# Performance work log

Hardware: AMD Instinct MI355X
Metric: run time of the kernel (lower is better)

The kernel has to match this reference:

```python
import jax, jax.numpy as jnp
import numpy as np

B, NW, NS, SL = 32, 500, 50, 40
EMB, HID, VOCAB, E = 300, 150, 50000, 563200
N = B * (NW + NS)
MAXPOS = 512


def _sinusoid(n_pos, d):
    pos = np.arange(n_pos)[:, None].astype(np.float64)
    i = np.arange(d)[None, :]
    ang = pos / np.power(10000.0, 2 * (i // 2) / d)
    tab = np.zeros((n_pos, d))
    tab[:, 0::2] = np.sin(ang[:, 0::2])
    tab[:, 1::2] = np.cos(ang[:, 1::2])
    tab[0] = 0.0  # padding_idx=0
    return jnp.asarray(tab, dtype=jnp.float32)

_POS_TAB = _sinusoid(MAXPOS + 1, EMB)


def setup_inputs():
    keys = iter(jax.random.split(jax.random.key(0), 48))
    def nrm(shape, s=0.05):
        return jax.random.normal(next(keys), shape, dtype=jnp.float32) * s
    inp = {}
    inp["x"] = jax.random.randint(next(keys), (B, NW), 0, VOCAB, dtype=jnp.int32)
    inp["sent_x"] = jax.random.randint(next(keys), (B, NS, SL), 0, VOCAB, dtype=jnp.int32)
    inp["edge_index"] = jax.random.randint(next(keys), (2, E), 0, N, dtype=jnp.int32)
    inp["embed_table"] = nrm((VOCAB, EMB)).at[0].set(0.0)  # padding_idx=0
    for h in range(2, 8):
        inp["conv_w%d" % h] = nrm((50, 1, h, EMB))
        inp["conv_b%d" % h] = nrm((50,))
    inp["cnn_proj_w"] = nrm((HID, EMB)); inp["cnn_proj_b"] = nrm((HID,))
    inp["lstm_w_ih_l0"] = nrm((2, 4 * HID, HID)); inp["lstm_w_hh_l0"] = nrm((2, 4 * HID, HID))
    inp["lstm_b_ih_l0"] = nrm((2, 4 * HID)); inp["lstm_b_hh_l0"] = nrm((2, 4 * HID))
    inp["lstm_w_ih_l1"] = nrm((2, 4 * HID, 2 * HID)); inp["lstm_w_hh_l1"] = nrm((2, 4 * HID, HID))
    inp["lstm_b_ih_l1"] = nrm((2, 4 * HID)); inp["lstm_b_hh_l1"] = nrm((2, 4 * HID))
    inp["lstm_proj_w"] = nrm((HID, 2 * HID)); inp["lstm_proj_b"] = nrm((HID,))
    inp["gc0_w"] = nrm((HID, EMB)); inp["gc0_b"] = nrm((HID,))
    inp["gc1_w"] = nrm((HID, HID)); inp["gc1_b"] = nrm((HID,))
    inp["gc2_w"] = nrm((HID, HID)); inp["gc2_b"] = nrm((HID,))
    return inp


def _forward(x, sent_x, edge_index, embed_table, conv_ws, conv_bs,
             cnn_proj_w, cnn_proj_b, w_ih0, w_hh0, b_ih0, b_hh0,
             w_ih1, w_hh1, b_ih1, b_hh1, lstm_proj_w, lstm_proj_b,
             gc0_w, gc0_b, gc1_w, gc1_b, gc2_w, gc2_b):
    Bsz, S, L = sent_x.shape
    Nn = Bsz * S
    emb_words = embed_table[x]                                   # [B, NW, EMB]
    tok = embed_table[sent_x].reshape(Nn, L, EMB)                # [Nn, L, EMB]
    sentlen = (sent_x != 0).sum(-1).reshape(Nn)                  # token count per sentence
    a = jnp.arange(L)
    input_pos = jnp.where(a[None, :] < sentlen[:, None], a[None, :] + 1, 0)
    enc = tok + _POS_TAB[input_pos]
    # CNN ngram features: conv heights 2..7, full-width kernels == windowed matmuls
    feats = []
    for w, b in zip(conv_ws, conv_bs):
        h = w.shape[2]
        acc = b + sum(jnp.einsum('nld,od->nlo', enc[:, k:L - h + 1 + k, :], w[:, 0, k, :]) for k in range(h))
        feats.append(jnp.max(jax.nn.relu(acc), axis=1))          # [Nn, 50]
    ngram = jnp.concatenate(feats, axis=1)                        # [Nn, 300]
    snode_pos = jnp.tile(jnp.arange(S), Bsz)
    cnn_feat = ((ngram + _POS_TAB[snode_pos]) @ cnn_proj_w.T + cnn_proj_b).reshape(Bsz, S, HID)
    glen = (sent_x[:, :, 0] != 0).sum(-1)                         # valid sentence count per graph

    def lstm_dir(xs, w_ih, w_hh, bias):
        def step(carry, xt):
            hh, cc = carry
            g = xt @ w_ih.T + hh @ w_hh.T + bias
            i, f, gg, o = jnp.split(g, 4, axis=-1)
            cc = jax.nn.sigmoid(f) * cc + jax.nn.sigmoid(i) * jnp.tanh(gg)
            hh = jax.nn.sigmoid(o) * jnp.tanh(cc)
            return (hh, cc), hh
        z = jnp.zeros((xs.shape[0], HID), xs.dtype)
        _, hs = jax.lax.scan(step, (z, z), jnp.swapaxes(xs, 0, 1))
        return jnp.swapaxes(hs, 0, 1)

    def rev_within(xs):
        # reverse only the first glen[b] steps (packed-sequence semantics)
        T = xs.shape[1]; t = jnp.arange(T)
        idx = jnp.where(t[None, :] < glen[:, None], glen[:, None] - 1 - t[None, :], t[None, :])
        return jnp.take_along_axis(xs, idx[:, :, None], axis=1)

    def bidir(xs, w_ih, w_hh, b_i, b_h):
        f = lstm_dir(xs, w_ih[0], w_hh[0], b_i[0] + b_h[0])
        r = rev_within(lstm_dir(rev_within(xs), w_ih[1], w_hh[1], b_i[1] + b_h[1]))
        return jnp.concatenate([f, r], axis=-1)

    h1 = bidir(cnn_feat, w_ih0, w_hh0, b_ih0, b_hh0)
    h2 = bidir(h1, w_ih1, w_hh1, b_ih1, b_hh1)
    mask = (jnp.arange(S)[None, :] < glen[:, None]).astype(h2.dtype)[:, :, None]
    lstm_feat = (h2 * mask) @ lstm_proj_w.T + lstm_proj_b
    sent_out = jnp.concatenate([cnn_feat, lstm_feat], axis=-1)    # [B, S, 300]
    nodes = jnp.concatenate([emb_words, sent_out], axis=1)        # [B, NW+S, 300]
    nodes = (nodes @ gc0_w.T + gc0_b).reshape(-1, HID)            # [N, 150]
    Nt = nodes.shape[0]
    loop = jnp.arange(Nt, dtype=edge_index.dtype)
    src = jnp.concatenate([edge_index[0], loop])                  # add self-loops
    dst = jnp.concatenate([edge_index[1], loop])
    deg = jax.ops.segment_sum(jnp.ones(src.shape[0], nodes.dtype), dst, num_segments=Nt)
    dis = jnp.where(deg > 0, jax.lax.rsqrt(deg), 0.0)
    norm = (dis[src] * dis[dst])[:, None]

    def gcn(xin, w, bias):
        xw = xin @ w.T
        return jax.ops.segment_sum(xw[src] * norm, dst, num_segments=Nt) + bias

    h = jax.nn.elu(gcn(nodes, gc1_w, gc1_b))
    # F.dropout with training=False -> identity
    return gcn(h, gc2_w, gc2_b), emb_words


def reference(x, sent_x, edge_index, embed_table, conv_w2, conv_b2, conv_w3, conv_b3,
              conv_w4, conv_b4, conv_w5, conv_b5, conv_w6, conv_b6, conv_w7, conv_b7,
              cnn_proj_w, cnn_proj_b, lstm_w_ih_l0, lstm_w_hh_l0, lstm_b_ih_l0, lstm_b_hh_l0,
              lstm_w_ih_l1, lstm_w_hh_l1, lstm_b_ih_l1, lstm_b_hh_l1, lstm_proj_w, lstm_proj_b,
              gc0_w, gc0_b, gc1_w, gc1_b, gc2_w, gc2_b):
    conv_ws = [conv_w2, conv_w3, conv_w4, conv_w5, conv_w6, conv_w7]
    conv_bs = [conv_b2, conv_b3, conv_b4, conv_b5, conv_b6, conv_b7]
    return _forward(x, sent_x, edge_index, embed_table, conv_ws, conv_bs,
                    cnn_proj_w, cnn_proj_b, lstm_w_ih_l0, lstm_w_hh_l0, lstm_b_ih_l0, lstm_b_hh_l0,
                    lstm_w_ih_l1, lstm_w_hh_l1, lstm_b_ih_l1, lstm_b_hh_l1, lstm_proj_w, lstm_proj_b,
                    gc0_w, gc0_b, gc1_w, gc1_b, gc2_w, gc2_b)
```

## Files before the change

### kernel.cpp

```cpp
#include <hip/hip_runtime.h>
#include <stdint.h>
#include <math.h>

#define EDGES 563200
#define NNODES 17600
#define OUT0SZ 2640000
#define MROWS 64000
#define MPAD  64016
#define KSTRIDE 2112

typedef _Float16 h2 __attribute__((ext_vector_type(2)));
typedef _Float16 h4 __attribute__((ext_vector_type(4)));
typedef _Float16 v8h __attribute__((ext_vector_type(8)));
typedef float v4f __attribute__((ext_vector_type(4)));

__device__ __forceinline__ float sigm(float x){ return 1.f / (1.f + expf(-x)); }

__device__ __forceinline__ float fdot2_(h2 a, h2 b, float c){
#if __has_builtin(__builtin_amdgcn_fdot2)
  return __builtin_amdgcn_fdot2(a, b, c, false);
#else
  return c + (float)a.x * (float)b.x + (float)a.y * (float)b.y;
#endif
}

__global__ void gcnk_postab(float* __restrict__ pos){
  int idx = blockIdx.x * 256 + threadIdx.x;
  if (idx >= 513 * 300) return;
  int p = idx / 300, i = idx - p * 300;
  float v = 0.f;
  if (p != 0){
    double expo = (double)(2 * (i / 2)) / 300.0;
    double ang = (double)p / pow(10000.0, expo);
    v = (float)((i & 1) ? cos(ang) : sin(ang));
  }
  pos[idx] = v;
}

__global__ void gcnk_prep(const int* __restrict__ sx, int* __restrict__ sentlen,
                          int* __restrict__ glen){
  int tid = blockIdx.x * 256 + threadIdx.x;
  if (tid < 1600){
    int c = 0;
    for (int j = 0; j < 40; j++) c += (sx[tid * 40 + j] != 0);
    sentlen[tid] = c;
  } else if (tid < 1632){
    int b = tid - 1600, c = 0;
    for (int s = 0; s < 50; s++) c += (sx[b * 2000 + s * 40] != 0);
    glen[b] = c;
  }
}

__global__ void gcnk_rowmap(const int* __restrict__ glen, int* __restrict__ rowmap){
  int i = blockIdx.x * 256 + threadIdx.x;
  if (i >= 1600) return;
  int b = i / 50, t = i - b * 50, g = glen[b];
  rowmap[i] = b * 50 + ((t < g) ? (g - 1 - t) : t);
}

__global__ void gcnk_embw(const int* __restrict__ x, const float* __restrict__ tab,
                          float4* __restrict__ out){
  int idx = blockIdx.x * 256 + threadIdx.x;
  if (idx >= 16000 * 75) return;
  int row = idx / 75, q = idx - row * 75;
  const float4* t = (const float4*)tab;
  out[idx] = t[x[row] * 75 + q];
}

__global__ void gcnk_zeroi(unsigned int* __restrict__ p, int n){
  int i = blockIdx.x * 256 + threadIdx.x;
  if (i < n) p[i] = 0u;
}

__global__ void gcnk_ench(const int* __restrict__ sx, const float* __restrict__ tab,
                          const float* __restrict__ pos, const int* __restrict__ sentlen,
                          _Float16* __restrict__ ench){
  int idx = blockIdx.x * 256 + threadIdx.x;
  if (idx >= MPAD * 75) return;
  int row = idx / 75, q = idx - row * 75;
  int d = q * 4;
  h4 o; o[0] = (_Float16)0.f; o[1] = (_Float16)0.f; o[2] = (_Float16)0.f; o[3] = (_Float16)0.f;
  if (row < MROWS){
    int n = row / 40, l = row - n * 40;
    int tok = sx[n * 40 + l];
    int p = (l < sentlen[n]) ? (l + 1) : 0;
    float4 a = *(const float4*)(tab + (size_t)tok * 300 + d);
    float4 b = *(const float4*)(pos + (size_t)p * 300 + d);
    o[0] = (_Float16)(a.x + b.x); o[1] = (_Float16)(a.y + b.y);
    o[2] = (_Float16)(a.z + b.z); o[3] = (_Float16)(a.w + b.w);
  }
  *(h4*)(ench + (size_t)row * 300 + d) = o;
}

__global__ void gcnk_bpack(const float* w2, const float* w3, const float* w4,
                           const float* w5, const float* w6, const float* w7,
                           const float* c2, const float* c3, const float* c4,
                           const float* c5, const float* c6, const float* c7,
                           _Float16* __restrict__ Bp, float* __restrict__ bias_p){
  int idx = blockIdx.x * 256 + threadIdx.x;
  if (idx < 2 * 160 * KSTRIDE){
    int n = idx / KSTRIDE, kk = idx - n * KSTRIDE;
    int g = n / 160, c = n - g * 160;
    _Float16 v = (_Float16)0.f;
    if (c < 150){
      int H = 3 * g + 2 + c / 50, o = c % 50;
      if (kk < 300 * H){
        const float* w;
        switch (H){ case 2: w = w2; break; case 3: w = w3; break;
                    case 4: w = w4; break; case 5: w = w5; break;
                    case 6: w = w6; break; default: w = w7; break; }
        v = (_Float16)w[o * 300 * H + kk];
      }
    }
    Bp[idx] = v;
  }
  if (idx < 320){
    int g = idx / 160, c = idx - g * 160;
    float bv = 0.f;
    if (c < 150){
      int H = 3 * g + 2 + c / 50, o = c % 50;
      const float* cbp;
      switch (H){ case 2: cbp = c2; break; case 3: cbp = c3; break;
                  case 4: cbp = c4; break; case 5: cbp = c5; break;
                  case 6: cbp = c6; break; default: cbp = c7; break; }
      bv = cbp[o];
    }
    bias_p[idx] = bv;
  }
}

__global__ __launch_bounds__(256)
void gcnk_convmfma(const _Float16* __restrict__ A, const _Float16* __restrict__ Bp,
                   const float* __restrict__ bias_p, unsigned int* __restrict__ ngram_u){
  __shared__ __align__(16) char smem[23040];
  _Float16* As = (_Float16*)smem;
  _Float16* Bs = (_Float16*)(smem + 10240);
  float* Cs = (float*)smem;
  const int tid = threadIdx.x;
  const int m0 = blockIdx.x * 128;
  const int grp = blockIdx.y;
  const _Float16* Bg = Bp + (size_t)grp * 160 * KSTRIDE;
  const int kmax = grp ? 2112 : 1216;
  const int w = tid >> 6, lane = tid & 63;
  const int wm = (w >> 1) * 64, wn = (w & 1) * 80;
  const int fm = lane & 15, fq = lane >> 4;
  v4f acc[4][5] = {};

  for (int kc = 0; kc < kmax; kc += 32){
    #pragma unroll
    for (int j = 0; j < 4; j++){
      int u = tid + 256 * j;
      int row = u >> 3, part = u & 7;
      uint2 v = *(const uint2*)(A + (size_t)(m0 + row) * 300 + kc + part * 4);
      *(uint2*)(As + row * 40 + part * 4) = v;
    }
    #pragma unroll
    for (int j = 0; j < 5; j++){
      int u = tid + 256 * j;
      int row = u >> 3, part = u & 7;
      uint2 v = *(const uint2*)(Bg + (size_t)row * KSTRIDE + kc + part * 4);
      *(uint2*)(Bs + row * 40 + part * 4) = v;
    }
    __syncthreads();
    v8h af[4], bf[5];
    #pragma unroll
    for (int mt = 0; mt < 4; mt++)
      af[mt] = *(const v8h*)(As + (wm + mt * 16 + fm) * 40 + fq * 8);
    #pragma unroll
    for (int nt = 0; nt < 5; nt++)
      bf[nt] = *(const v8h*)(Bs + (wn + nt * 16 + fm) * 40 + fq * 8);
    #pragma unroll
    for (int mt = 0; mt < 4; mt++)
      #pragma unroll
      for (int nt = 0; nt < 5; nt++)
        acc[mt][nt] = __builtin_amdgcn_mfma_f32_16x16x32_f16(af[mt], bf[nt], acc[mt][nt], 0, 0, 0);
    __syncthreads();
  }

  for (int p = 0; p < 5; p++){
    __syncthreads();
    #pragma unroll
    for (int nt = 0; nt < 5; nt++){
      int cstart = wn + nt * 16;
      if ((cstart >> 5) == p){
        int co = cstart - p * 32 + fm;
        #pragma unroll
        for (int mt = 0; mt < 4; mt++)
          #pragma unroll
          for (int r = 0; r < 4; r++)
            Cs[(wm + mt * 16 + fq * 4 + r) * 33 + co] = acc[mt][nt][r];
      }
    }
    __syncthreads();
    if (tid < 128){
      int cl = tid & 31, si = tid >> 5;
      int col = p * 32 + cl;
      if (col < 150){
        int H = 3 * grp + 2 + col / 50, lh = 41 - H;
        int sent = m0 / 40 + si;
        int rlo = sent * 40; if (rlo < m0) rlo = m0;
        int rhi = sent * 40 + lh; if (rhi > m0 + 128) rhi = m0 + 128;
        if (rlo < rhi){
          float bv = bias_p[grp * 160 + col];
          float vmax = 0.f;
          for (int r = rlo; r < rhi; r++){
            float v = Cs[(r - m0) * 33 + cl] + bv;
            vmax = fmaxf(vmax, v);
          }
          atomicMax(ngram_u + sent * 300 + grp * 150 + col, __float_as_uint(vmax));
        }
      }
    }
  }
}

__global__ void gcnk_addpos(float* __restrict__ ngram, const float* __restrict__ pos){
  int idx = blockIdx.x * 256 + threadIdx.x;
  if (idx >= 1600 * 300) return;
  int row = idx / 300, d = idx - row * 300;
  ngram[idx] += pos[(row % 50) * 300 + d];
}

template<int BM, int BN, int WMT, int WNT>
__global__ __launch_bounds__(256)
void gcnk_mgemm(const float* __restrict__ A, const float* __restrict__ Wt,
                const float* __restrict__ b1, const float* __restrict__ b2,
                float* __restrict__ C, int M, int N, int K){
  __shared__ __align__(16) _Float16 As[BM * 40];
  __shared__ __align__(16) _Float16 Bs[BN * 40];
  const int tid = threadIdx.x;
  const int m0 = blockIdx.x * BM, n0 = blockIdx.y * BN;
  const int w = tid >> 6, lane = tid & 63;
  const int wm = (w >> 1) * (WMT * 16), wn = (w & 1) * (WNT * 16);
  const int fm = lane & 15, fq = lane >> 4;
  v4f acc[WMT][WNT] = {};
  const int nch = (K + 31) >> 5;
  for (int ch = 0; ch < nch; ch++){
    int kc = ch * 32;
    #pragma unroll
    for (int j = 0; j < BM / 64; j++){
      int u = tid + 256 * j;
      int row = u >> 2, cb = (u & 3) * 8;
      int gm = m0 + row, gk = kc + cb;
      v8h vv;
      if (gm < M && gk + 8 <= K){
        const float* p = A + (size_t)gm * K + gk;
        #pragma unroll
        for (int e = 0; e < 8; e++) vv[e] = (_Float16)p[e];
      } else {
        #pragma unroll
        for (int e = 0; e < 8; e++)
          vv[e] = (gm < M && gk + e < K) ? (_Float16)A[(size_t)gm * K + gk + e] : (_Float16)0.f;
      }
      *(v8h*)(As + row * 40 + cb) = vv;
    }
    {
      int row = tid >> 2, cb = (tid & 3) * 8;
      int gn = n0 + row, gk = kc + cb;
      v8h vv;
      if (gn < N && gk + 8 <= K){
        const float* p = Wt + (size_t)gn * K + gk;
        #pragma unroll
        for (int e = 0; e < 8; e++) vv[e] = (_Float16)p[e];
      } else {
        #pragma unroll
        for (int e = 0; e < 8; e++)
          vv[e] = (gn < N && gk + e < K) ? (_Float16)Wt[(size_t)gn * K + gk + e] : (_Float16)0.f;
      }
      *(v8h*)(Bs + row * 40 + cb) = vv;
    }
    __syncthreads();
    v8h af[WMT], bf[WNT];
    #pragma unroll
    for (int mt = 0; mt < WMT; mt++)
      af[mt] = *(const v8h*)(As + (wm + mt * 16 + fm) * 40 + fq * 8);
    #pragma unroll
    for (int nt = 0; nt < WNT; nt++)
      bf[nt] = *(const v8h*)(Bs + (wn + nt * 16 + fm) * 40 + fq * 8);
    #pragma unroll
    for (int mt = 0; mt < WMT; mt++)
      #pragma unroll
      for (int nt = 0; nt < WNT; nt++)
        acc[mt][nt] = __builtin_amdgcn_mfma_f32_16x16x32_f16(af[mt], bf[nt], acc[mt][nt], 0, 0, 0);
    __syncthreads();
  }
  #pragma unroll
  for (int nt = 0; nt < WNT; nt++){
    int gn = n0 + wn + nt * 16 + fm;
    if (gn >= N) continue;
    float badd = (b1 ? b1[gn] : 0.f) + (b2 ? b2[gn] : 0.f);
    #pragma unroll
    for (int mt = 0; mt < WMT; mt++)
      #pragma unroll
      for (int r = 0; r < 4; r++){
        int gm = m0 + wm + mt * 16 + fq * 4 + r;
        if (gm < M) C[(size_t)gm * N + gn] = acc[mt][nt][r] + badd;
      }
  }
}

__global__ void gcnk_permute150(float* __restrict__ dst, const float* __restrict__ src,
                                const int* __restrict__ map){
  int idx = blockIdx.x * 256 + threadIdx.x;
  if (idx >= 1600 * 150) return;
  int row = idx / 150, d = idx - row * 150;
  dst[idx] = src[map[row] * 150 + d];
}

__global__ void gcnk_concat(float* __restrict__ dst, const float* __restrict__ A,
                            const float* __restrict__ Bs, const int* __restrict__ mapA,
                            const int* __restrict__ mapB, const int* __restrict__ glen,
                            int usemask){
  int idx = blockIdx.x * 256 + threadIdx.x;
  if (idx >= 1600 * 300) return;
  int row = idx / 300, d = idx - row * 300;
  int b = row / 50, t = row - b * 50;
  float v;
  if (d < 150){ int r = mapA ? mapA[row] : row; v = A[r * 150 + d]; }
  else        { int r = mapB ? mapB[row] : row; v = Bs[r * 150 + d - 150]; }
  if (usemask && t >= glen[b]) v = 0.f;
  dst[idx] = v;
}

__global__ void gcnk_whhpack(const float* __restrict__ whh, _Float16* __restrict__ wpad){
  int idx = blockIdx.x * 256 + threadIdx.x;
  if (idx >= 1200 * 152) return;
  int row = idx / 152, col = idx - row * 152;
  wpad[idx] = (col < 150) ? (_Float16)whh[row * 150 + col] : (_Float16)0.f;
}

__global__ __launch_bounds__(640)
void gcnk_lstm(const float* __restrict__ xf, const float* __restrict__ xr,
               const _Float16* __restrict__ wpad, float* __restrict__ fo,
               float* __restrict__ ro){
  int b = blockIdx.x >> 1, dir = blockIdx.x & 1;
  const float* xih = dir ? xr : xf;
  float* out = dir ? ro : fo;
  __shared__ __align__(16) _Float16 hh[160];
  __shared__ float gates[600];
  const int tid = threadIdx.x;

  h2 w[76];
  if (tid < 600){
    const h2* wrow = (const h2*)(wpad + ((size_t)dir * 600 + tid) * 152);
    #pragma unroll
    for (int j = 0; j < 76; j++) w[j] = wrow[j];
  }
  for (int u = tid; u < 160; u += 640) hh[u] = (_Float16)0.f;
  float creg = 0.f;
  __syncthreads();

  for (int t = 0; t < 50; t++){
    if (tid < 600){
      float acc = xih[(b * 50 + t) * 600 + tid];
      #pragma unroll
      for (int j = 0; j < 19; j++){
        union { float4 f; h2 h[4]; } u;
        u.f = *(const float4*)(hh + j * 8);
        acc = fdot2_(w[4 * j + 0], u.h[0], acc);
        acc = fdot2_(w[4 * j + 1], u.h[1], acc);
        acc = fdot2_(w[4 * j + 2], u.h[2], acc);
        acc = fdot2_(w[4 * j + 3], u.h[3], acc);
      }
      gates[tid] = acc;
    }
    __syncthreads();
    if (tid < 150){
      float ig = sigm(gates[tid]);
      float fg = sigm(gates[150 + tid]);
      float gg = tanhf(gates[300 + tid]);
      float og = sigm(gates[450 + tid]);
      creg = fg * creg + ig * gg;
      float hn = og * tanhf(creg);
      hh[tid] = (_Float16)hn;
      out[(b * 50 + t) * 150 + tid] = hn;
    }
    __syncthreads();
  }
}

__global__ void gcnk_nodes_in(const int* __restrict__ x, const float* __restrict__ tab,
                              const float* __restrict__ cnnf, const float* __restrict__ lstmf,
                              float* __restrict__ out){
  int idx = blockIdx.x * 256 + threadIdx.x;
  if (idx >= NNODES * 300) return;
  int nrow = idx / 300, d = idx - nrow * 300;
  int b = nrow / 550, j = nrow - b * 550;
  float v;
  if (j < 500) v = tab[x[b * 500 + j] * 300 + d];
  else {
    int r = b * 50 + (j - 500);
    v = (d < 150) ? cnnf[r * 150 + d] : lstmf[r * 150 + d - 150];
  }
  out[idx] = v;
}

__global__ void gcnk_hist(const int* __restrict__ ei, int* __restrict__ ecnt){
  int e = blockIdx.x * 256 + threadIdx.x;
  if (e < EDGES) atomicAdd(&ecnt[ei[EDGES + e]], 1);
}

__global__ __launch_bounds__(1024)
void gcnk_scan(const int* __restrict__ ecnt, int* __restrict__ eoff,
               int* __restrict__ ecur){
  __shared__ int buf[1024];
  int tid = threadIdx.x;
  int running = 0;
  for (int c = 0; c < 18; c++){
    int i = c * 1024 + tid;
    int v = (i < NNODES) ? ecnt[i] : 0;
    buf[tid] = v;
    __syncthreads();
    for (int s = 1; s < 1024; s <<= 1){
      int t2 = (tid >= s) ? buf[tid - s] : 0;
      __syncthreads();
      buf[tid] += t2;
      __syncthreads();
    }
    int excl = running + buf[tid] - v;
    int tot = buf[1023];
    if (i < NNODES){ eoff[i] = excl; ecur[i] = excl; }
    running += tot;
    __syncthreads();
  }
}

__global__ void gcnk_scatter(const int* __restrict__ ei, int* __restrict__ ecur,
                             int* __restrict__ esrc){
  int e = blockIdx.x * 256 + threadIdx.x;
  if (e < EDGES){
    int d = ei[EDGES + e];
    int p = atomicAdd(&ecur[d], 1);
    esrc[p] = ei[e];
  }
}

__global__ void gcnk_dis2(const int* __restrict__ ecnt, float* __restrict__ dis){
  int i = blockIdx.x * 256 + threadIdx.x;
  if (i < NNODES) dis[i] = rsqrtf((float)(ecnt[i] + 1));
}

__global__ __launch_bounds__(128)
void gcnk_aggcsr(const int* __restrict__ eoff, const int* __restrict__ ecnt,
                 const int* __restrict__ esrc, const float* __restrict__ dis,
                 const float* __restrict__ xw, float* __restrict__ agg){
  int d = blockIdx.x, t = threadIdx.x;
  float dd = dis[d];
  const float* xd = xw + (size_t)d * 150;
  float a0 = xd[t] * dd;
  float a1 = (t < 22) ? xd[128 + t] * dd : 0.f;
  int beg = eoff[d], end = beg + ecnt[d];
  for (int j = beg; j < end; j++){
    int s = esrc[j];
    float ds = dis[s];
    const float* xs = xw + (size_t)s * 150;
    a0 += xs[t] * ds;
    if (t < 22) a1 += xs[128 + t] * ds;
  }
  agg[(size_t)d * 150 + t] = a0 * dd;
  if (t < 22) agg[(size_t)d * 150 + 128 + t] = a1 * dd;
}

__global__ void gcnk_elu(float* __restrict__ h, const float* __restrict__ agg,
                         const float* __restrict__ bias){
  int idx = blockIdx.x * 256 + threadIdx.x;
  if (idx >= NNODES * 150) return;
  int c = idx % 150;
  float v = agg[idx] + bias[c];
  h[idx] = (v > 0.f) ? v : expm1f(v);
}

__global__ void gcnk_out0(float* __restrict__ out, const float* __restrict__ agg,
                          const float* __restrict__ bias){
  int idx = blockIdx.x * 256 + threadIdx.x;
  if (idx >= NNODES * 150) return;
  int c = idx % 150;
  out[idx] = agg[idx] + bias[c];
}

extern "C" void kernel_launch(void* const* d_in, const int* in_sizes, int n_in,
                              void* d_out, int out_size, void* d_ws, size_t ws_size,
                              hipStream_t stream){
  (void)in_sizes; (void)n_in; (void)out_size; (void)ws_size;

  char* wsb = (char*)d_ws;
  size_t off = 0;
  auto alloc = [&](size_t bytes) -> void* {
    void* p = wsb + off;
    off = (off + bytes + 255) & ~(size_t)255;
    return p;
  };
  float* pos_tab  = (float*)alloc(513 * 300 * 4);
  int*   sentlen  = (int*)alloc(1600 * 4);
  int*   glen     = (int*)alloc(32 * 4);
  int*   rowmap   = (int*)alloc(1600 * 4);
  float* ngram    = (float*)alloc(1600 * 300 * 4);
  float* cnn_feat = (float*)alloc(1600 * 150 * 4);
  float* cnn_rev  = (float*)alloc(1600 * 150 * 4);
  float* xih_f    = (float*)alloc(1600 * 600 * 4);
  float* xih_r    = (float*)alloc(1600 * 600 * 4);
  float* f0       = (float*)alloc(1600 * 150 * 4);
  float* r0       = (float*)alloc(1600 * 150 * 4);
  float* f1       = (float*)alloc(1600 * 150 * 4);
  float* r1       = (float*)alloc(1600 * 150 * 4);
  float* h1       = (float*)alloc(1600 * 300 * 4);
  float* h1rev    = (float*)alloc(1600 * 300 * 4);
  float* hm       = (float*)alloc(1600 * 300 * 4);
  float* lstm_ft  = (float*)alloc(1600 * 150 * 4);
  float* nodes_in = (float*)alloc((size_t)NNODES * 300 * 4);
  float* nodes    = (float*)alloc((size_t)NNODES * 150 * 4);
  float* dis      = (float*)alloc(NNODES * 4);
  float* xw       = (float*)alloc((size_t)NNODES * 150 * 4);
  float* agg      = (float*)alloc((size_t)NNODES * 150 * 4);
  _Float16* ench  = (_Float16*)alloc((size_t)MPAD * 300 * 2);
  _Float16* Bp    = (_Float16*)alloc((size_t)2 * 160 * KSTRIDE * 2);
  float* bias_p   = (float*)alloc(320 * 4);
  _Float16* wpad0 = (_Float16*)alloc(1200 * 152 * 2);
  _Float16* wpad1 = (_Float16*)alloc(1200 * 152 * 2);
  int*   ecnt     = (int*)alloc(NNODES * 4);
  int*   eoff     = (int*)alloc(NNODES * 4);
  int*   ecur     = (int*)alloc(NNODES * 4);
  int*   esrc     = (int*)alloc(EDGES * 4);

  const int*   x   = (const int*)d_in[0];
  const int*   sx  = (const int*)d_in[1];
  const int*   ei  = (const int*)d_in[2];
  const float* tab = (const float*)d_in[3];
  const float *cw[6], *cb[6];
  for (int h = 0; h < 6; h++){ cw[h] = (const float*)d_in[4 + 2 * h]; cb[h] = (const float*)d_in[5 + 2 * h]; }
  const float* cnnw = (const float*)d_in[16]; const float* cnnb = (const float*)d_in[17];
  const float* wih0 = (const float*)d_in[18]; const float* whh0 = (const float*)d_in[19];
  const float* bih0 = (const float*)d_in[20]; const float* bhh0 = (const float*)d_in[21];
  const float* wih1 = (const float*)d_in[22]; const float* whh1 = (const float*)d_in[23];
  const float* bih1 = (const float*)d_in[24]; const float* bhh1 = (const float*)d_in[25];
  const float* lpw  = (const float*)d_in[26]; const float* lpb  = (const float*)d_in[27];
  const float* g0w  = (const float*)d_in[28]; const float* g0b  = (const float*)d_in[29];
  const float* g1w  = (const float*)d_in[30]; const float* g1b  = (const float*)d_in[31];
  const float* g2w  = (const float*)d_in[32]; const float* g2b  = (const float*)d_in[33];

  float* out0 = (float*)d_out;
  float4* out1 = (float4*)((float*)d_out + OUT0SZ);

  auto mgemmL = [&](const float* A, const float* W, const float* b1, const float* b2,
                    float* C, int M, int N, int K){
    dim3 g((M + 127) / 128, (N + 63) / 64);
    gcnk_mgemm<128, 64, 4, 2><<<g, 256, 0, stream>>>(A, W, b1, b2, C, M, N, K);
  };
  auto mgemmS = [&](const float* A, const float* W, const float* b1, const float* b2,
                    float* C, int M, int N, int K){
    dim3 g((M + 63) / 64, (N + 63) / 64);
    gcnk_mgemm<64, 64, 2, 2><<<g, 256, 0, stream>>>(A, W, b1, b2, C, M, N, K);
  };

  gcnk_postab<<<602, 256, 0, stream>>>(pos_tab);
  gcnk_prep<<<7, 256, 0, stream>>>(sx, sentlen, glen);
  gcnk_rowmap<<<7, 256, 0, stream>>>(glen, rowmap);
  gcnk_embw<<<4688, 256, 0, stream>>>(x, tab, out1);

  gcnk_zeroi<<<1875, 256, 0, stream>>>((unsigned int*)ngram, 1600 * 300);
  gcnk_ench<<<(MPAD * 75 + 255) / 256, 256, 0, stream>>>(sx, tab, pos_tab, sentlen, ench);
  gcnk_bpack<<<(2 * 160 * KSTRIDE + 255) / 256, 256, 0, stream>>>(
      cw[0], cw[1], cw[2], cw[3], cw[4], cw[5],
      cb[0], cb[1], cb[2], cb[3], cb[4], cb[5], Bp, bias_p);
  gcnk_whhpack<<<713, 256, 0, stream>>>(whh0, wpad0);
  gcnk_whhpack<<<713, 256, 0, stream>>>(whh1, wpad1);
  {
    dim3 g(500, 2);
    gcnk_convmfma<<<g, 256, 0, stream>>>(ench, Bp, bias_p, (unsigned int*)ngram);
  }
  gcnk_addpos<<<1875, 256, 0, stream>>>(ngram, pos_tab);
  mgemmS(ngram, cnnw, cnnb, nullptr, cnn_feat, 1600, 150, 300);

  gcnk_permute150<<<938, 256, 0, stream>>>(cnn_rev, cnn_feat, rowmap);
  mgemmS(cnn_feat, wih0,             bih0,       bhh0,       xih_f, 1600, 600, 150);
  mgemmS(cnn_rev,  wih0 + 600 * 150, bih0 + 600, bhh0 + 600, xih_r, 1600, 600, 150);
  gcnk_lstm<<<64, 640, 0, stream>>>(xih_f, xih_r, wpad0, f0, r0);

  gcnk_concat<<<1875, 256, 0, stream>>>(h1,    f0, r0, nullptr, rowmap, glen, 0);
  gcnk_concat<<<1875, 256, 0, stream>>>(h1rev, f0, r0, rowmap, nullptr, glen, 0);
  mgemmS(h1,    wih1,             bih1,       bhh1,       xih_f, 1600, 600, 300);
  mgemmS(h1rev, wih1 + 600 * 300, bih1 + 600, bhh1 + 600, xih_r, 1600, 600, 300);
  gcnk_lstm<<<64, 640, 0, stream>>>(xih_f, xih_r, wpad1, f1, r1);

  gcnk_concat<<<1875, 256, 0, stream>>>(hm, f1, r1, nullptr, rowmap, glen, 1);
  mgemmS(hm, lpw, lpb, nullptr, lstm_ft, 1600, 150, 300);

  gcnk_nodes_in<<<20625, 256, 0, stream>>>(x, tab, cnn_feat, lstm_ft, nodes_in);
  mgemmL(nodes_in, g0w, g0b, nullptr, nodes, NNODES, 150, 300);

  gcnk_zeroi<<<69, 256, 0, stream>>>((unsigned int*)ecnt, NNODES);
  gcnk_hist<<<2200, 256, 0, stream>>>(ei, ecnt);
  gcnk_scan<<<1, 1024, 0, stream>>>(ecnt, eoff, ecur);
  gcnk_scatter<<<2200, 256, 0, stream>>>(ei, ecur, esrc);
  gcnk_dis2<<<69, 256, 0, stream>>>(ecnt, dis);

  mgemmL(nodes, g1w, nullptr, nullptr, xw, NNODES, 150, 150);
  gcnk_aggcsr<<<NNODES, 128, 0, stream>>>(eoff, ecnt, esrc, dis, xw, agg);
  gcnk_elu<<<10313, 256, 0, stream>>>(nodes, agg, g1b);

  mgemmL(nodes, g2w, nullptr, nullptr, xw, NNODES, 150, 150);
  gcnk_aggcsr<<<NNODES, 128, 0, stream>>>(eoff, ecnt, esrc, dis, xw, agg);
  gcnk_out0<<<10313, 256, 0, stream>>>(out0, agg, g2b);
}
```

Before: 901.1 us.

## Restructure conv GEMM, fuse GCN bias/ELU into fp16 aggregation, warp-shuffle scan

Several independent changes land together. The conv MFMA kernel now loads its whole 64-row A tile into shared memory once and streams B fragments directly from global memory with register double-buffering, on twice as many blocks. The GCN feature transform writes fp16 with a 160-column stride, and the CSR aggregation reads half2 values and applies bias and ELU inline, which removes the separate elu and out0 kernels and the fp32 intermediate buffers. The prefix scan becomes a per-thread serial scan plus a wavefront shuffle scan, and the LSTM dot product is split across four accumulators. Storing GCN intermediates in fp16 adds precision risk, and the larger shared-memory footprint in the conv kernel may lower occupancy.

```diff
diff --git a/kernel.cpp b/kernel.cpp
--- a/kernel.cpp
+++ b/kernel.cpp
@@ -132,49 +132,59 @@
 __global__ __launch_bounds__(256)
 void gcnk_convmfma(const _Float16* __restrict__ A, const _Float16* __restrict__ Bp,
                    const float* __restrict__ bias_p, unsigned int* __restrict__ ngram_u){
-  __shared__ __align__(16) char smem[23040];
-  _Float16* As = (_Float16*)smem;
-  _Float16* Bs = (_Float16*)(smem + 10240);
+  __shared__ __align__(16) char smem[45056];
   float* Cs = (float*)smem;
   const int tid = threadIdx.x;
-  const int m0 = blockIdx.x * 128;
+  const int m0 = blockIdx.x * 64;
   const int grp = blockIdx.y;
   const _Float16* Bg = Bp + (size_t)grp * 160 * KSTRIDE;
   const int kmax = grp ? 2112 : 1216;
   const int w = tid >> 6, lane = tid & 63;
-  const int wm = (w >> 1) * 64, wn = (w & 1) * 80;
+  const int wm = (w >> 1) * 32, wn = (w & 1) * 80;
   const int fm = lane & 15, fq = lane >> 4;
-  v4f acc[4][5] = {};
-
-  for (int kc = 0; kc < kmax; kc += 32){
-    #pragma unroll
-    for (int j = 0; j < 4; j++){
-      int u = tid + 256 * j;
-      int row = u >> 3, part = u & 7;
-      uint2 v = *(const uint2*)(A + (size_t)(m0 + row) * 300 + kc + part * 4);
-      *(uint2*)(As + row * 40 + part * 4) = v;
-    }
-    #pragma unroll
-    for (int j = 0; j < 5; j++){
-      int u = tid + 256 * j;
-      int row = u >> 3, part = u & 7;
-      uint2 v = *(const uint2*)(Bg + (size_t)row * KSTRIDE + kc + part * 4);
-      *(uint2*)(Bs + row * 40 + part * 4) = v;
-    }
-    __syncthreads();
-    v8h af[4], bf[5];
-    #pragma unroll
-    for (int mt = 0; mt < 4; mt++)
-      af[mt] = *(const v8h*)(As + (wm + mt * 16 + fm) * 40 + fq * 8);
-    #pragma unroll
-    for (int nt = 0; nt < 5; nt++)
-      bf[nt] = *(const v8h*)(Bs + (wn + nt * 16 + fm) * 40 + fq * 8);
-    #pragma unroll
-    for (int mt = 0; mt < 4; mt++)
-      #pragma unroll
-      for (int nt = 0; nt < 5; nt++)
-        acc[mt][nt] = __builtin_amdgcn_mfma_f32_16x16x32_f16(af[mt], bf[nt], acc[mt][nt], 0, 0, 0);
-    __syncthreads();
+
+  {
+    const uint4* gp = (const uint4*)(A + (size_t)m0 * 300);
+    uint4* lp = (uint4*)smem;
+    #pragma unroll
+    for (int j = 0; j < 11; j++)
+      lp[j * 256 + tid] = gp[j * 256 + tid];
+  }
+  __syncthreads();
+
+  v4f acc[2][5] = {};
+  const _Float16* bptr[5];
+  #pragma unroll
+  for (int nt = 0; nt < 5; nt++)
+    bptr[nt] = Bg + (size_t)(wn + nt * 16 + fm) * KSTRIDE + fq * 8;
+  const int aoff0 = (wm + fm) * 600 + fq * 16;
+  const int aoff1 = aoff0 + 16 * 600;
+
+  auto loadB = [&](v8h* dst, int k){
+    #pragma unroll
+    for (int nt = 0; nt < 5; nt++) dst[nt] = *(const v8h*)(bptr[nt] + k);
+  };
+  auto step = [&](int kc2, v8h* bf){
+    const char* p0 = smem + aoff0 + kc2 * 2;
+    const char* p1 = smem + aoff1 + kc2 * 2;
+    union { uint2 u[2]; v8h v; } a0, a1;
+    a0.u[0] = *(const uint2*)p0; a0.u[1] = *(const uint2*)(p0 + 8);
+    a1.u[0] = *(const uint2*)p1; a1.u[1] = *(const uint2*)(p1 + 8);
+    #pragma unroll
+    for (int nt = 0; nt < 5; nt++){
+      acc[0][nt] = __builtin_amdgcn_mfma_f32_16x16x32_f16(a0.v, bf[nt], acc[0][nt], 0, 0, 0);
+      acc[1][nt] = __builtin_amdgcn_mfma_f32_16x16x32_f16(a1.v, bf[nt], acc[1][nt], 0, 0, 0);
+    }
+  };
+
+  v8h bX[5], bY[5];
+  loadB(bX, 0);
+  loadB(bY, 32);
+  for (int kc = 0; kc < kmax; kc += 64){
+    step(kc, bX);
+    if (kc + 64 < kmax) loadB(bX, kc + 64);
+    step(kc + 32, bY);
+    if (kc + 96 < kmax) loadB(bY, kc + 96);
   }
 
   for (int p = 0; p < 5; p++){
@@ -185,29 +195,31 @@
       if ((cstart >> 5) == p){
         int co = cstart - p * 32 + fm;
         #pragma unroll
-        for (int mt = 0; mt < 4; mt++)
+        for (int mt = 0; mt < 2; mt++)
           #pragma unroll
           for (int r = 0; r < 4; r++)
             Cs[(wm + mt * 16 + fq * 4 + r) * 33 + co] = acc[mt][nt][r];
       }
     }
     __syncthreads();
-    if (tid < 128){
+    if (tid < 96){
       int cl = tid & 31, si = tid >> 5;
       int col = p * 32 + cl;
       if (col < 150){
         int H = 3 * grp + 2 + col / 50, lh = 41 - H;
         int sent = m0 / 40 + si;
-        int rlo = sent * 40; if (rlo < m0) rlo = m0;
-        int rhi = sent * 40 + lh; if (rhi > m0 + 128) rhi = m0 + 128;
-        if (rlo < rhi){
-          float bv = bias_p[grp * 160 + col];
-          float vmax = 0.f;
-          for (int r = rlo; r < rhi; r++){
-            float v = Cs[(r - m0) * 33 + cl] + bv;
-            vmax = fmaxf(vmax, v);
+        if (sent < 1600){
+          int rlo = sent * 40; if (rlo < m0) rlo = m0;
+          int rhi = sent * 40 + lh; if (rhi > m0 + 64) rhi = m0 + 64;
+          if (rlo < rhi){
+            float bv = bias_p[grp * 160 + col];
+            float vmax = 0.f;
+            for (int r = rlo; r < rhi; r++){
+              float v = Cs[(r - m0) * 33 + cl] + bv;
+              vmax = fmaxf(vmax, v);
+            }
+            atomicMax(ngram_u + sent * 300 + grp * 150 + col, __float_as_uint(vmax));
           }
-          atomicMax(ngram_u + sent * 300 + grp * 150 + col, __float_as_uint(vmax));
         }
       }
     }
@@ -221,11 +233,11 @@
   ngram[idx] += pos[(row % 50) * 300 + d];
 }
 
-template<int BM, int BN, int WMT, int WNT>
+template<int BM, int BN, int WMT, int WNT, int OUTH>
 __global__ __launch_bounds__(256)
 void gcnk_mgemm(const float* __restrict__ A, const float* __restrict__ Wt,
                 const float* __restrict__ b1, const float* __restrict__ b2,
-                float* __restrict__ C, int M, int N, int K){
+                void* __restrict__ Cv, int M, int N, int K){
   __shared__ __align__(16) _Float16 As[BM * 40];
   __shared__ __align__(16) _Float16 Bs[BN * 40];
   const int tid = threadIdx.x;
@@ -294,7 +306,11 @@
       #pragma unroll
       for (int r = 0; r < 4; r++){
         int gm = m0 + wm + mt * 16 + fq * 4 + r;
-        if (gm < M) C[(size_t)gm * N + gn] = acc[mt][nt][r] + badd;
+        if (gm < M){
+          float val = acc[mt][nt][r] + badd;
+          if (OUTH) ((_Float16*)Cv)[(size_t)gm * 160 + gn] = (_Float16)val;
+          else      ((float*)Cv)[(size_t)gm * N + gn] = val;
+        }
       }
   }
 }
@@ -353,16 +369,17 @@
   for (int t = 0; t < 50; t++){
     if (tid < 600){
       float acc = xih[(b * 50 + t) * 600 + tid];
+      float a0 = 0.f, a1 = 0.f, a2 = 0.f, a3 = 0.f;
       #pragma unroll
       for (int j = 0; j < 19; j++){
         union { float4 f; h2 h[4]; } u;
         u.f = *(const float4*)(hh + j * 8);
-        acc = fdot2_(w[4 * j + 0], u.h[0], acc);
-        acc = fdot2_(w[4 * j + 1], u.h[1], acc);
-        acc = fdot2_(w[4 * j + 2], u.h[2], acc);
-        acc = fdot2_(w[4 * j + 3], u.h[3], acc);
+        a0 = fdot2_(w[4 * j + 0], u.h[0], a0);
+        a1 = fdot2_(w[4 * j + 1], u.h[1], a1);
+        a2 = fdot2_(w[4 * j + 2], u.h[2], a2);
+        a3 = fdot2_(w[4 * j + 3], u.h[3], a3);
       }
-      gates[tid] = acc;
+      gates[tid] = acc + ((a0 + a1) + (a2 + a3));
     }
     __syncthreads();
     if (tid < 150){
@@ -403,25 +420,40 @@
 __global__ __launch_bounds__(1024)
 void gcnk_scan(const int* __restrict__ ecnt, int* __restrict__ eoff,
                int* __restrict__ ecur){
-  __shared__ int buf[1024];
+  __shared__ int wsum[16];
   int tid = threadIdx.x;
-  int running = 0;
-  for (int c = 0; c < 18; c++){
-    int i = c * 1024 + tid;
-    int v = (i < NNODES) ? ecnt[i] : 0;
-    buf[tid] = v;
-    __syncthreads();
-    for (int s = 1; s < 1024; s <<= 1){
-      int t2 = (tid >= s) ? buf[tid - s] : 0;
-      __syncthreads();
-      buf[tid] += t2;
-      __syncthreads();
-    }
-    int excl = running + buf[tid] - v;
-    int tot = buf[1023];
-    if (i < NNODES){ eoff[i] = excl; ecur[i] = excl; }
-    running += tot;
-    __syncthreads();
+  int base = tid * 18;
+  int pre[18];
+  int s = 0;
+  #pragma unroll
+  for (int i = 0; i < 18; i++){
+    int idx = base + i;
+    int c = (idx < NNODES) ? ecnt[idx] : 0;
+    pre[i] = s; s += c;
+  }
+  int lane = tid & 63, wid = tid >> 6;
+  int run = s;
+  #pragma unroll
+  for (int off = 1; off < 64; off <<= 1){
+    int y = __shfl_up(run, off, 64);
+    if (lane >= off) run += y;
+  }
+  if (lane == 63) wsum[wid] = run;
+  __syncthreads();
+  if (tid == 0){
+    int a = 0;
+    #pragma unroll
+    for (int i = 0; i < 16; i++){ int t2 = wsum[i]; wsum[i] = a; a += t2; }
+  }
+  __syncthreads();
+  int excl = wsum[wid] + run - s;
+  #pragma unroll
+  for (int i = 0; i < 18; i++){
+    int idx = base + i;
+    if (idx < NNODES){
+      int e = excl + pre[i];
+      eoff[idx] = e; ecur[idx] = e;
+    }
   }
 }
 
@@ -441,41 +473,36 @@
 }
 
 __global__ __launch_bounds__(128)
-void gcnk_aggcsr(const int* __restrict__ eoff, const int* __restrict__ ecnt,
-                 const int* __restrict__ esrc, const float* __restrict__ dis,
-                 const float* __restrict__ xw, float* __restrict__ agg){
+void gcnk_aggcsr_h(const int* __restrict__ eoff, const int* __restrict__ ecnt,
+                   const int* __restrict__ esrc, const float* __restrict__ dis,
+                   const _Float16* __restrict__ xw, const float* __restrict__ bias,
+                   float* __restrict__ out, int doelu){
   int d = blockIdx.x, t = threadIdx.x;
   float dd = dis[d];
-  const float* xd = xw + (size_t)d * 150;
-  float a0 = xd[t] * dd;
-  float a1 = (t < 22) ? xd[128 + t] * dd : 0.f;
+  bool act = t < 75;
+  float ax = 0.f, ay = 0.f;
+  if (act){
+    h2 v = *(const h2*)(xw + (size_t)d * 160 + 2 * t);
+    ax = (float)v[0] * dd; ay = (float)v[1] * dd;
+  }
   int beg = eoff[d], end = beg + ecnt[d];
   for (int j = beg; j < end; j++){
     int s = esrc[j];
-    float ds = dis[s];
-    const float* xs = xw + (size_t)s * 150;
-    a0 += xs[t] * ds;
-    if (t < 22) a1 += xs[128 + t] * ds;
-  }
-  agg[(size_t)d * 150 + t] = a0 * dd;
-  if (t < 22) agg[(size_t)d * 150 + 128 + t] = a1 * dd;
-}
-
-__global__ void gcnk_elu(float* __restrict__ h, const float* __restrict__ agg,
-                         const float* __restrict__ bias){
-  int idx = blockIdx.x * 256 + threadIdx.x;
-  if (idx >= NNODES * 150) return;
-  int c = idx % 150;
-  float v = agg[idx] + bias[c];
-  h[idx] = (v > 0.f) ? v : expm1f(v);
-}
-
-__global__ void gcnk_out0(float* __restrict__ out, const float* __restrict__ agg,
-                          const float* __restrict__ bias){
-  int idx = blockIdx.x * 256 + threadIdx.x;
-  if (idx >= NNODES * 150) return;
-  int c = idx % 150;
-  out[idx] = agg[idx] + bias[c];
+    float ds_ = dis[s];
+    if (act){
+      h2 v = *(const h2*)(xw + (size_t)s * 160 + 2 * t);
+      ax += (float)v[0] * ds_; ay += (float)v[1] * ds_;
+    }
+  }
+  if (act){
+    float o0 = ax * dd + bias[2 * t];
+    float o1 = ay * dd + bias[2 * t + 1];
+    if (doelu){
+      o0 = (o0 > 0.f) ? o0 : expm1f(o0);
+      o1 = (o1 > 0.f) ? o1 : expm1f(o1);
+    }
+    *(float2*)(out + (size_t)d * 150 + 2 * t) = make_float2(o0, o1);
+  }
 }
 
 extern "C" void kernel_launch(void* const* d_in, const int* in_sizes, int n_in,
@@ -510,8 +537,7 @@
   float* nodes_in = (float*)alloc((size_t)NNODES * 300 * 4);
   float* nodes    = (float*)alloc((size_t)NNODES * 150 * 4);
   float* dis      = (float*)alloc(NNODES * 4);
-  float* xw       = (float*)alloc((size_t)NNODES * 150 * 4);
-  float* agg      = (float*)alloc((size_t)NNODES * 150 * 4);
+  _Float16* xwh   = (_Float16*)alloc((size_t)NNODES * 160 * 2);
   _Float16* ench  = (_Float16*)alloc((size_t)MPAD * 300 * 2);
   _Float16* Bp    = (_Float16*)alloc((size_t)2 * 160 * KSTRIDE * 2);
   float* bias_p   = (float*)alloc(320 * 4);
@@ -542,14 +568,18 @@
   float4* out1 = (float4*)((float*)d_out + OUT0SZ);
 
   auto mgemmL = [&](const float* A, const float* W, const float* b1, const float* b2,
-                    float* C, int M, int N, int K){
+                    void* C, int M, int N, int K){
     dim3 g((M + 127) / 128, (N + 63) / 64);
-    gcnk_mgemm<128, 64, 4, 2><<<g, 256, 0, stream>>>(A, W, b1, b2, C, M, N, K);
+    gcnk_mgemm<128, 64, 4, 2, 0><<<g, 256, 0, stream>>>(A, W, b1, b2, C, M, N, K);
+  };
+  auto mgemmLH = [&](const float* A, const float* W, void* C, int M, int N, int K){
+    dim3 g((M + 127) / 128, (N + 63) / 64);
+    gcnk_mgemm<128, 64, 4, 2, 1><<<g, 256, 0, stream>>>(A, W, nullptr, nullptr, C, M, N, K);
   };
   auto mgemmS = [&](const float* A, const float* W, const float* b1, const float* b2,
-                    float* C, int M, int N, int K){
+                    void* C, int M, int N, int K){
     dim3 g((M + 63) / 64, (N + 63) / 64);
-    gcnk_mgemm<64, 64, 2, 2><<<g, 256, 0, stream>>>(A, W, b1, b2, C, M, N, K);
+    gcnk_mgemm<64, 64, 2, 2, 0><<<g, 256, 0, stream>>>(A, W, b1, b2, C, M, N, K);
   };
 
   gcnk_postab<<<602, 256, 0, stream>>>(pos_tab);
@@ -565,7 +595,7 @@
   gcnk_whhpack<<<713, 256, 0, stream>>>(whh0, wpad0);
   gcnk_whhpack<<<713, 256, 0, stream>>>(whh1, wpad1);
   {
-    dim3 g(500, 2);
+    dim3 g(1000, 2);
     gcnk_convmfma<<<g, 256, 0, stream>>>(ench, Bp, bias_p, (unsigned int*)ngram);
   }
   gcnk_addpos<<<1875, 256, 0, stream>>>(ngram, pos_tab);
@@ -594,11 +624,9 @@
   gcnk_scatter<<<2200, 256, 0, stream>>>(ei, ecur, esrc);
   gcnk_dis2<<<69, 256, 0, stream>>>(ecnt, dis);
 
-  mgemmL(nodes, g1w, nullptr, nullptr, xw, NNODES, 150, 150);
-  gcnk_aggcsr<<<NNODES, 128, 0, stream>>>(eoff, ecnt, esrc, dis, xw, agg);
-  gcnk_elu<<<10313, 256, 0, stream>>>(nodes, agg, g1b);
-
-  mgemmL(nodes, g2w, nullptr, nullptr, xw, NNODES, 150, 150);
-  gcnk_aggcsr<<<NNODES, 128, 0, stream>>>(eoff, ecnt, esrc, dis, xw, agg);
-  gcnk_out0<<<10313, 256, 0, stream>>>(out0, agg, g2b);
-}
+  mgemmLH(nodes, g1w, xwh, NNODES, 150, 150);
+  gcnk_aggcsr_h<<<NNODES, 128, 0, stream>>>(eoff, ecnt, esrc, dis, xwh, g1b, nodes, 1);
+
+  mgemmLH(nodes, g2w, xwh, NNODES, 150, 150);
+  gcnk_aggcsr_h<<<NNODES, 128, 0, stream>>>(eoff, ecnt, esrc, dis, xwh, g2b, out0, 0);
+}
```

After: 972.4 us. 7.9% more time.
